# Kernel optimization log

Hardware: AMD Instinct MI355X
Metric: run time of the kernel (lower is better)

## Reference

```python
import jax, jax.numpy as jnp
import numpy as np

M1, M2, BS = 2000, 400, 8
AT = M1 + M2
E1, E2, E3 = 60000, 20000, 20000
H, F, NG, L, C = 64, 64, 50, 4, 4
CUTOFF = 10.0
LOG2 = 0.6931471805599453  # shift of ShiftedSoftplus


def _ssp(x):
    return jax.nn.softplus(x) - LOG2


def _smear(d):
    # GaussianSmearing(0, cutoff, NG)
    offset = jnp.linspace(0.0, CUTOFF, NG)
    coeff = -0.5 / (offset[1] - offset[0]) ** 2
    return jnp.exp(coeff * (d[:, None] - offset[None, :]) ** 2)  # [E, NG]


def _colored_mlp(attr, colors, w1, b1, w2, b2):
    # w1:[C,NG,F] b1:[C,F] w2:[C,F,F] b2:[C,F]; route each edge through its color's MLP
    out = jnp.zeros((attr.shape[0], w1.shape[-1]), attr.dtype)
    for c in range(C):  # fixed small color count
        h = _ssp(attr @ w1[c] + b1[c]) @ w2[c] + b2[c]
        out = out + jnp.where((colors == c)[:, None], h, jnp.zeros((), attr.dtype))
    return out


def _block(h, ei, ew, attr, col, p):
    # InteractionBlock: CFConv -> ssp -> linear
    mw1, mb1, mw2, mb2, cw1, cw2, cb2, bw, bb = p
    Ccut = 0.5 * (jnp.cos(ew * jnp.pi / CUTOFF) + 1.0)
    W = _colored_mlp(attr, col, mw1, mb1, mw2, mb2) * Ccut[:, None]  # [E,F]
    x = h @ cw1                                   # lin1 (no bias) [N,F]
    msg = x[ei[:, 0]] * W                         # gather x_j, modulate
    agg = jax.ops.segment_sum(msg, ei[:, 1], num_segments=h.shape[0])  # scatter-add
    x = agg @ cw2 + cb2                           # lin2
    return _ssp(x) @ bw + bb                      # act + block linear


def _batch_graph(ei, ew, col):
    # replicate per-structure edges across the batch with node offset b*AT
    offs = (jnp.arange(BS, dtype=ei.dtype) * AT)[:, None, None]
    ei_b = (ei[None] + offs).reshape(-1, 2)
    return ei_b, jnp.tile(ew, BS), jnp.tile(col, BS)


def _forward(sites, sites_p, e1, ew1, c1, e2, ew2, c2, e3, ew3, c3,
             emb_w, emb_p_w, mlp_w1, mlp_b1, mlp_w2, mlp_b2,
             conv_w1, conv_w2, conv_b2, blk_w, blk_b,
             out_w1, out_b1, out_w2, out_b2):
    h = jnp.concatenate([emb_w[sites], emb_p_w[sites_p]], axis=1).reshape(BS * AT, H)
    graphs = []
    for (ei, ew, col) in ((e1, ew1, c1), (e2, ew2, c2), (e3, ew3, c3)):
        ei_b, ew_b, col_b = _batch_graph(ei, ew, col)
        graphs.append((ei_b, ew_b, col_b, _smear(ew_b)))
    for l in range(L):
        delta = jnp.zeros_like(h)
        for g, (ei_b, ew_b, col_b, attr_b) in enumerate(graphs):
            p = (mlp_w1[l, g], mlp_b1[l, g], mlp_w2[l, g], mlp_b2[l, g],
                 conv_w1[l, g], conv_w2[l, g], conv_b2[l, g], blk_w[l, g], blk_b[l, g])
            delta = delta + _block(h, ei_b, ew_b, attr_b, col_b, p)
        h = h + delta
    hp = h.reshape(BS, AT, H)[:, M1:, :]   # mask selects pore nodes only
    o = hp @ out_w1 + out_b1               # NB: original has `h - self.act(h)` no-op, so no activation here
    o = o @ out_w2 + out_b2                # [BS, M2, 1]
    return o.sum(axis=1)                   # 'add' readout per batch -> [BS, 1]


def setup_inputs() -> dict:
    key = jax.random.key(0)
    ks = jax.random.split(key, 24)
    f = lambda i, shape, s=0.1: jax.random.normal(ks[i], shape, jnp.float32) * s
    sites = jax.random.randint(ks[0], (BS, M1), 0, 1, dtype=jnp.int32)
    sites_p = jax.random.randint(ks[1], (BS, M2), 0, 2, dtype=jnp.int32)
    e1 = jax.random.randint(ks[2], (E1, 2), 0, M1, dtype=jnp.int32)
    e2 = jnp.stack([jax.random.randint(ks[3], (E2,), 0, M1, dtype=jnp.int32),
                    jax.random.randint(ks[4], (E2,), M1, AT, dtype=jnp.int32)], 1)
    e3 = jnp.stack([jax.random.randint(ks[5], (E3,), M1, AT, dtype=jnp.int32),
                    jax.random.randint(ks[6], (E3,), 0, M1, dtype=jnp.int32)], 1)
    ew1 = jax.random.uniform(ks[7], (E1,), jnp.float32, 0.5, CUTOFF)
    ew2 = jax.random.uniform(ks[8], (E2,), jnp.float32, 0.5, CUTOFF)
    ew3 = jax.random.uniform(ks[9], (E3,), jnp.float32, 0.5, CUTOFF)
    c1 = jax.random.randint(ks[10], (E1,), 0, C, dtype=jnp.int32)
    c2 = jax.random.randint(ks[11], (E2,), 0, C, dtype=jnp.int32)
    c3 = jax.random.randint(ks[12], (E3,), 0, C, dtype=jnp.int32)
    return {
        'sites': sites, 'sites_p': sites_p,
        'edge_idx1': e1, 'edge_weight1': ew1, 'colors1': c1,
        'edge_idx2': e2, 'edge_weight2': ew2, 'colors2': c2,
        'edge_idx3': e3, 'edge_weight3': ew3, 'colors3': c3,
        'emb_w': f(13, (1, H), 1.0), 'emb_p_w': f(14, (2, H), 1.0),
        'mlp_w1': f(15, (L, 3, C, NG, F)), 'mlp_b1': jnp.zeros((L, 3, C, F), jnp.float32),
        'mlp_w2': f(16, (L, 3, C, F, F)), 'mlp_b2': jnp.zeros((L, 3, C, F), jnp.float32),
        'conv_w1': f(17, (L, 3, H, F)), 'conv_w2': f(18, (L, 3, F, H)),
        'conv_b2': jnp.zeros((L, 3, H), jnp.float32),
        'blk_w': f(19, (L, 3, H, H)), 'blk_b': jnp.zeros((L, 3, H), jnp.float32),
        'out_w1': f(20, (H, H // 2)), 'out_b1': jnp.zeros((H // 2,), jnp.float32),
        'out_w2': f(21, (H // 2, 1)), 'out_b2': jnp.zeros((1,), jnp.float32),
    }


def reference(sites, sites_p, edge_idx1, edge_weight1, colors1,
              edge_idx2, edge_weight2, colors2, edge_idx3, edge_weight3, colors3,
              emb_w, emb_p_w, mlp_w1, mlp_b1, mlp_w2, mlp_b2,
              conv_w1, conv_w2, conv_b2, blk_w, blk_b,
              out_w1, out_b1, out_w2, out_b2):
    return _forward(sites, sites_p, edge_idx1, edge_weight1, colors1,
                    edge_idx2, edge_weight2, colors2, edge_idx3, edge_weight3, colors3,
                    emb_w, emb_p_w, mlp_w1, mlp_b1, mlp_w2, mlp_b2,
                    conv_w1, conv_w2, conv_b2, blk_w, blk_b,
                    out_w1, out_b1, out_w2, out_b2)
```

## Files before the change

### kernel.cpp

```cpp
#include <hip/hip_runtime.h>
#include <math.h>

constexpr int M1 = 2000, M2 = 400, BS = 8;
constexpr int AT = M1 + M2;
constexpr int NN = BS * AT;
constexpr int E1 = 60000, E2 = 20000, E3 = 20000;
constexpr int ET = E1 + E2 + E3;
constexpr int H = 64, F = 64, NG = 50, L = 4, C = 4;
constexpr float CUTOFF = 10.0f;
constexpr float LOG2F_ = 0.6931471805599453f;

constexpr float SMEAR_STEP = 10.0f / 49.0f;
constexpr float SMEAR_COEFF = -12.005f;
constexpr float PI_OVER_CUT = 0.31415926535897932f;

constexpr int NBLK = (ET + 255) / 256;

constexpr int NT = 256;
constexpr float DSCALE = (float)(NT - 1) / CUTOFF;

constexpr int TILE_M = 32;

constexpr int SITE_T = M1 / 4;
constexpr int PORE_T = M2 / 4;
constexpr int NBLK_L = 2 * (SITE_T + PORE_T);

constexpr int LT0 = M1 / 4;
constexpr int LT1 = M1 / 4;
constexpr int LT2 = M2 / 4;
constexpr int LTOT = LT0 + LT1 + LT2;

constexpr int A_TAB  = 192;
constexpr int A_INIT = NN * 64 / 256;
constexpr int A_CNT  = NBLK;
constexpr int A_CV   = 3;
constexpr int A_TOT  = A_TAB + A_INIT + A_CNT + A_CV;
constexpr int B_PACK = 48 * NT * 64 / 256;
constexpr int B_TOT  = B_PACK + 3 + 2;

constexpr size_t O_HA    = 0;
constexpr size_t O_HB    = O_HA  + (size_t)NN * 64 * 4;
constexpr size_t O_XG    = O_HB  + (size_t)NN * 64 * 4;
constexpr size_t O_DG    = O_XG  + (size_t)3 * AT * 512 * 2;
constexpr size_t O_TAB2  = O_DG  + (size_t)3 * NN * 64 * 4;
constexpr size_t O_EDATA = O_TAB2 + (size_t)48 * NT * 64 * 4;
constexpr size_t O_INT   = O_EDATA + (size_t)ET * 16;
constexpr int I_DEG  = 0;
constexpr int I_CUR  = 7200;
constexpr int I_ZEND = 14400;
constexpr int I_BASE = 14400;
constexpr int I_PERM = 21616;
constexpr int I_CV   = 26016;

__device__ inline float sspf(float x) {
    return fmaxf(x, 0.0f) + log1pf(expf(-fabsf(x))) - LOG2F_;
}
__device__ inline float sspf_fast(float x) {
    float t = __expf(-fabsf(x));
    return fmaxf(x, 0.0f) + __logf(1.0f + t) - LOG2F_;
}

__device__ inline unsigned int bf16rn(float x) {
    unsigned int u = __float_as_uint(x);
    u = (u + 0x7FFFu + ((u >> 16) & 1u)) >> 16;
    return u & 0xFFFFu;
}

__device__ inline int graph_off(int g) { return g == 0 ? 0 : (g == 1 ? E1 : E1 + E2); }

__device__ inline void edge_decode(int idx, int& g, int& e,
                                   const int* ei1, const int* ei2, const int* ei3,
                                   const int* c1, const int* c2, const int* c3,
                                   const int*& ei, const int*& cl) {
    if (idx < E1)            { g = 0; e = idx;           ei = ei1; cl = c1; }
    else if (idx < E1 + E2)  { g = 1; e = idx - E1;      ei = ei2; cl = c2; }
    else                     { g = 2; e = idx - E1 - E2; ei = ei3; cl = c3; }
}

__global__ __launch_bounds__(256) void k_setupA(
    const float* __restrict__ mlp_w1, const float* __restrict__ mlp_b1,
    const float* __restrict__ mlp_w2, const float* __restrict__ mlp_b2,
    float* __restrict__ tabF,
    const int* __restrict__ sites, const int* __restrict__ sites_p,
    const float* __restrict__ emb_w, const float* __restrict__ emb_p_w,
    float* __restrict__ h,
    const int* __restrict__ ei1, const int* __restrict__ ei2,
    const int* __restrict__ ei3, const int* __restrict__ c1,
    const int* __restrict__ c2, const int* __restrict__ c3,
    int* __restrict__ deg,
    const float* __restrict__ conv_b2, const float* __restrict__ blk_w,
    const float* __restrict__ blk_b, float* __restrict__ cvbuf) {
    int bid = blockIdx.x;
    int t = threadIdx.x;
    if (bid < A_TAB) {
        const int lane = t & 63;
        int wslot = bid * 4 + (t >> 6);
        int s = wslot >> 4;
        int pq = wslot & 15;
        int l = s % L;
        int gc = s / L;
        int c = gc % C;
        int g = gc / C;
        size_t wb = (size_t)((l * 3 + g) * C + c);
        const float* w1 = mlp_w1 + wb * NG * F;
        const float* w2 = mlp_w2 + wb * F * F;
        float w1c[NG], w2c[F];
        #pragma unroll
        for (int k = 0; k < NG; k++) w1c[k] = w1[k * F + lane];
        #pragma unroll
        for (int k = 0; k < F; k++) w2c[k] = w2[k * F + lane];
        float b1c = mlp_b1[wb * F + lane];
        float b2c = mlp_b2[wb * F + lane];
        for (int pp = 0; pp < 16; pp++) {
            int p = pq * 16 + pp;
            float d = (float)p * (CUTOFF / (float)(NT - 1));
            float dd = d - (float)lane * SMEAR_STEP;
            float av = (lane < NG) ? __expf(SMEAR_COEFF * dd * dd) : 0.0f;
            float acc = b1c;
            #pragma unroll
            for (int k = 0; k < NG; k++) acc = fmaf(__shfl(av, k), w1c[k], acc);
            float tt = sspf_fast(acc);
            float acc2 = b2c;
            #pragma unroll
            for (int j = 0; j < F; j++) acc2 = fmaf(__shfl(tt, j), w2c[j], acc2);
            float ccut = 0.5f * (__cosf(d * PI_OVER_CUT) + 1.0f);
            tabF[((size_t)s * NT + p) * 64 + lane] = acc2 * ccut;
        }
    } else if (bid < A_TAB + A_INIT) {
        int idx = (bid - A_TAB) * 256 + t;
        int f = idx & 63;
        int n = idx >> 6;
        int b = n / AT;
        int i = n - b * AT;
        float v;
        if (i < M1) v = emb_w[sites[b * M1 + i] * H + f];
        else        v = emb_p_w[sites_p[b * M2 + (i - M1)] * H + f];
        h[idx] = v;
    } else if (bid < A_TAB + A_INIT + A_CNT) {
        int idx = (bid - A_TAB - A_INIT) * 256 + t;
        if (idx < ET) {
            int g, e; const int* ei; const int* cl;
            edge_decode(idx, g, e, ei1, ei2, ei3, c1, c2, c3, ei, cl);
            atomicAdd(&deg[g * AT + ei[2 * e + 1]], 1);
        }
    } else {
        int s = (bid - A_TAB - A_INIT - A_CNT) * 4 + (t >> 6);
        int lane = t & 63;
        if (s < 12) {
            float sl = sspf(conv_b2[s * 64 + lane]);
            const float* bw = blk_w + (size_t)s * 4096;
            float a = blk_b[s * 64 + lane];
            #pragma unroll 8
            for (int k = 0; k < 64; k++)
                a = fmaf(__shfl(sl, k), bw[k * 64 + lane], a);
            cvbuf[s * 64 + lane] = a;
        }
    }
}

__global__ __launch_bounds__(256) void k_setupB(
    const float* __restrict__ tabF, unsigned int* __restrict__ tab2,
    const int* __restrict__ deg, int* __restrict__ base,
    int* __restrict__ perm) {
    int bid = blockIdx.x;
    int t = threadIdx.x;
    if (bid < B_PACK) {
        int idx = bid * 256 + t;
        int pc = idx & (NT * 64 - 1);
        int nxt = (pc < (NT - 1) * 64) ? idx + 64 : idx;
        unsigned int lo = bf16rn(tabF[idx]);
        unsigned int hi = bf16rn(tabF[nxt]);
        tab2[idx] = lo | (hi << 16);
    } else if (bid < B_PACK + 3) {
        const int T = 256, CH = 10;
        __shared__ int lsum[256];
        int g = bid - B_PACK;
        int loc[CH];
        int s = 0;
        #pragma unroll
        for (int i = 0; i < CH; i++) {
            int idx = t * CH + i;
            int v = (idx < AT) ? deg[g * AT + idx] : 0;
            loc[i] = s;
            s += v;
        }
        lsum[t] = s;
        __syncthreads();
        for (int off = 1; off < T; off <<= 1) {
            int v = 0;
            if (t >= off) v = lsum[t - off];
            __syncthreads();
            lsum[t] += v;
            __syncthreads();
        }
        int tb = lsum[t] - s;
        #pragma unroll
        for (int i = 0; i < CH; i++) {
            int idx = t * CH + i;
            if (idx < AT) base[g * (AT + 1) + idx] = tb + loc[i];
        }
        if (t == T - 1) base[g * (AT + 1) + AT] = lsum[T - 1];
    } else {
        __shared__ int hist[256];
        __shared__ int cur[256];
        int q = bid - B_PACK - 3;
        int cnt   = q ? M2 : M1;
        int obase = q ? M1 : 0;
        hist[t] = 0;
        __syncthreads();
        for (int i = t; i < cnt; i += 256) {
            int key = q ? deg[AT + M1 + i] : (deg[i] + deg[2 * AT + i]);
            atomicAdd(&hist[min(key, 255)], 1);
        }
        __syncthreads();
        if (t == 0) {
            int run = 0;
            for (int k = 0; k < 256; k++) { cur[k] = run; run += hist[k]; }
        }
        __syncthreads();
        for (int i = t; i < cnt; i += 256) {
            int key = q ? deg[AT + M1 + i] : (deg[i] + deg[2 * AT + i]);
            int pos = atomicAdd(&cur[min(key, 255)], 1);
            perm[obase + pos] = q ? (M1 + i) : i;
        }
    }
}

__device__ inline void fma4(float acc[4], float a, const float4 b) {
    acc[0] = fmaf(a, b.x, acc[0]);
    acc[1] = fmaf(a, b.y, acc[1]);
    acc[2] = fmaf(a, b.z, acc[2]);
    acc[3] = fmaf(a, b.w, acc[3]);
}

__device__ inline void stage_B(const float* __restrict__ gB, float (*Bs)[68], int t) {
    #pragma unroll
    for (int i = 0; i < 4; i++) {
        int v = t + i * 256;
        int r = v >> 4, c4 = (v & 15) * 4;
        *(float4*)&Bs[r][c4] = *(const float4*)(gB + (size_t)r * 64 + c4);
    }
}
__device__ inline void gemm_tile(const float (*As)[68], const float (*Bs)[68],
                                 int r0, int c0, float acc0[4], float acc1[4]) {
    #pragma unroll 4
    for (int k0 = 0; k0 < 64; k0 += 4) {
        float4 a0 = *(const float4*)&As[r0][k0];
        float4 a1 = *(const float4*)&As[r0 + 1][k0];
        float4 b0 = *(const float4*)&Bs[k0][c0];
        float4 b1 = *(const float4*)&Bs[k0 + 1][c0];
        float4 b2 = *(const float4*)&Bs[k0 + 2][c0];
        float4 b3 = *(const float4*)&Bs[k0 + 3][c0];
        fma4(acc0, a0.x, b0); fma4(acc0, a0.y, b1);
        fma4(acc0, a0.z, b2); fma4(acc0, a0.w, b3);
        fma4(acc1, a1.x, b0); fma4(acc1, a1.y, b1);
        fma4(acc1, a1.z, b2); fma4(acc1, a1.w, b3);
    }
}
__device__ inline void gemm_row(const float (*As)[68], const float (*Bs)[68],
                                int r, int c0, float acc[4]) {
    #pragma unroll 4
    for (int k0 = 0; k0 < 64; k0 += 4) {
        float4 a = *(const float4*)&As[r][k0];
        float4 b0 = *(const float4*)&Bs[k0][c0];
        float4 b1 = *(const float4*)&Bs[k0 + 1][c0];
        float4 b2 = *(const float4*)&Bs[k0 + 2][c0];
        float4 b3 = *(const float4*)&Bs[k0 + 3][c0];
        fma4(acc, a.x, b0); fma4(acc, a.y, b1);
        fma4(acc, a.z, b2); fma4(acc, a.w, b3);
    }
}

__device__ inline void xg_store8(const float (*T)[68],
                                 unsigned short* __restrict__ xg,
                                 int g, int i0, int t) {
    int k = t >> 6, c = t & 63;
    unsigned int w0 = bf16rn(T[k * 8 + 0][c]) | (bf16rn(T[k * 8 + 1][c]) << 16);
    unsigned int w1 = bf16rn(T[k * 8 + 2][c]) | (bf16rn(T[k * 8 + 3][c]) << 16);
    unsigned int w2 = bf16rn(T[k * 8 + 4][c]) | (bf16rn(T[k * 8 + 5][c]) << 16);
    unsigned int w3 = bf16rn(T[k * 8 + 6][c]) | (bf16rn(T[k * 8 + 7][c]) << 16);
    unsigned short* o0 = xg + (((size_t)(g * 2 + 0) * AT + i0 + k) * 64 + c) * 4;
    unsigned short* o1 = xg + (((size_t)(g * 2 + 1) * AT + i0 + k) * 64 + c) * 4;
    *(uint2*)o0 = make_uint2(w0, w1);
    *(uint2*)o1 = make_uint2(w2, w3);
}
__device__ inline void xg_store4(const float (*T)[68],
                                 unsigned short* __restrict__ xg,
                                 int g, int bh, const int* __restrict__ perm,
                                 int pbase, int gi, int t) {
    int k = t >> 6, c = t & 63;
    int node = perm[pbase + gi * 4 + k];
    unsigned int w0 = bf16rn(T[k * 4 + 0][c]) | (bf16rn(T[k * 4 + 1][c]) << 16);
    unsigned int w1 = bf16rn(T[k * 4 + 2][c]) | (bf16rn(T[k * 4 + 3][c]) << 16);
    unsigned short* out = xg + (((size_t)(g * 2 + bh) * AT + node) * 64 + c) * 4;
    *(uint2*)out = make_uint2(w0, w1);
}

__device__ inline float tab_lerp(unsigned int u, int z) {
    float lo = __uint_as_float(u << 16);
    float hi = __uint_as_float(u & 0xFFFF0000u);
    return fmaf(__int_as_float(z), hi - lo, lo);
}
__device__ inline void gmadd(float acc[4], uint2 q, float wl) {
    acc[0] = fmaf(__uint_as_float(q.x << 16),         wl, acc[0]);
    acc[1] = fmaf(__uint_as_float(q.x & 0xFFFF0000u), wl, acc[1]);
    acc[2] = fmaf(__uint_as_float(q.y << 16),         wl, acc[2]);
    acc[3] = fmaf(__uint_as_float(q.y & 0xFFFF0000u), wl, acc[3]);
}

__device__ inline void gather4(const int4* __restrict__ ed, int s, int e,
                               const unsigned int* __restrict__ tg,
                               const unsigned short* __restrict__ xgg,
                               int lane, float acc[4]) {
    int i = s;
    while (i < e) {
        int cnt = min(e - i, 64);
        int4 mrec = ed[i + min(lane, cnt - 1)];
        int j = 0;
        for (; j + 4 <= cnt; j += 4) {
            int x0 = __shfl(mrec.x, j),     y0 = __shfl(mrec.y, j),     z0 = __shfl(mrec.z, j);
            int x1 = __shfl(mrec.x, j + 1), y1 = __shfl(mrec.y, j + 1), z1 = __shfl(mrec.z, j + 1);
            int x2 = __shfl(mrec.x, j + 2), y2 = __shfl(mrec.y, j + 2), z2 = __shfl(mrec.z, j + 2);
            int x3 = __shfl(mrec.x, j + 3), y3 = __shfl(mrec.y, j + 3), z3 = __shfl(mrec.z, j + 3);
            unsigned int u0 = tg[(size_t)y0 * 64 + lane];
            unsigned int u1 = tg[(size_t)y1 * 64 + lane];
            unsigned int u2 = tg[(size_t)y2 * 64 + lane];
            unsigned int u3 = tg[(size_t)y3 * 64 + lane];
            uint2 q0 = *(const uint2*)(xgg + ((size_t)x0 << 8) + lane * 4);
            uint2 q1 = *(const uint2*)(xgg + ((size_t)x1 << 8) + lane * 4);
            uint2 q2 = *(const uint2*)(xgg + ((size_t)x2 << 8) + lane * 4);
            uint2 q3 = *(const uint2*)(xgg + ((size_t)x3 << 8) + lane * 4);
            float wl0 = tab_lerp(u0, z0);
            float wl1 = tab_lerp(u1, z1);
            float wl2 = tab_lerp(u2, z2);
            float wl3 = tab_lerp(u3, z3);
            gmadd(acc, q0, wl0); gmadd(acc, q1, wl1);
            gmadd(acc, q2, wl2); gmadd(acc, q3, wl3);
        }
        for (; j < cnt; j++) {
            int x0 = __shfl(mrec.x, j), y0 = __shfl(mrec.y, j), z0 = __shfl(mrec.z, j);
            unsigned int u0 = tg[(size_t)y0 * 64 + lane];
            uint2 q0 = *(const uint2*)(xgg + ((size_t)x0 << 8) + lane * 4);
            gmadd(acc, q0, tab_lerp(u0, z0));
        }
        i += cnt;
    }
}

__global__ __launch_bounds__(256) void k_layer(
    const int4* __restrict__ edata, const int* __restrict__ base,
    const int* __restrict__ perm,
    unsigned short* __restrict__ xg, const unsigned int* __restrict__ tab2,
    const float* __restrict__ conv_w2, const float* __restrict__ conv_b2,
    const float* __restrict__ blk_w, const float* __restrict__ blk_b,
    const float* __restrict__ conv_w1, const float* __restrict__ cvbuf,
    const float* __restrict__ hIn, float* __restrict__ hOut,
    int l, int last) {
    __shared__ float As[16][68];
    __shared__ float Ps[16][68];
    __shared__ float Bs[64][68];
    const int t = threadIdx.x;
    const int lane = t & 63;
    const int wv = t >> 6;
    int bid = blockIdx.x;
    int site, tile, bh;
    if (bid < 2 * SITE_T) { site = 1; tile = bid >> 1; bh = bid & 1; }
    else { site = 0; tile = (bid - 2 * SITE_T) >> 1; bh = (bid - 2 * SITE_T) & 1; }
    const int gi = site ? (SITE_T - 1 - tile) : (PORE_T - 1 - tile);
    const int pbperm = site ? 0 : M1;
    const int gA = site ? 0 : 1;
    const size_t pbA = (size_t)(l * 3 + gA);
    const size_t pbB = (size_t)(l * 3 + 2);

    stage_B(conv_w2 + pbA * 4096, Bs, t);

    const int dst = perm[pbperm + gi * 4 + wv];
    float accA[4] = {0, 0, 0, 0}, accB[4] = {0, 0, 0, 0};
    {
        int s = base[gA * (AT + 1) + dst];
        int e = base[gA * (AT + 1) + dst + 1];
        gather4(edata + graph_off(gA), s, e,
                tab2 + ((size_t)gA * C * L + l) * NT * 64,
                xg + (size_t)(gA * 2 + bh) * AT * 256, lane, accA);
    }
    if (site) {
        int s = base[2 * (AT + 1) + dst];
        int e = base[2 * (AT + 1) + dst + 1];
        gather4(edata + graph_off(2), s, e,
                tab2 + ((size_t)2 * C * L + l) * NT * 64,
                xg + (size_t)(2 * 2 + bh) * AT * 256, lane, accB);
    }
    #pragma unroll
    for (int b = 0; b < 4; b++) As[wv * 4 + b][lane] = accA[b];
    __syncthreads();

    const int r = t >> 4;
    const int c0 = (t & 15) * 4;
    const int k = r >> 2, bl = r & 3;
    const int node = perm[pbperm + gi * 4 + k];
    const int batch = bh * 4 + bl;
    const size_t o = ((size_t)batch * AT + node) * 64 + c0;
    const float* cvl = cvbuf + (size_t)l * 3 * 64;

    float4 cb = *(const float4*)(conv_b2 + pbA * 64 + c0);
    float x[4] = {cb.x, cb.y, cb.z, cb.w};
    gemm_row(As, Bs, r, c0, x);
    __syncthreads();
    *(float4*)&As[r][c0] =
        make_float4(sspf(x[0]), sspf(x[1]), sspf(x[2]), sspf(x[3]));
    stage_B(blk_w + pbA * 4096, Bs, t);
    __syncthreads();

    float4 hv = *(const float4*)(hIn + o);
    float4 bbA = *(const float4*)(blk_b + pbA * 64 + c0);
    float d[4];
    if (site) {
        float4 bbB = *(const float4*)(blk_b + pbB * 64 + c0);
        float4 cv1 = *(const float4*)(cvl + 64 + c0);
        d[0] = hv.x + bbA.x + bbB.x + cv1.x;
        d[1] = hv.y + bbA.y + bbB.y + cv1.y;
        d[2] = hv.z + bbA.z + bbB.z + cv1.z;
        d[3] = hv.w + bbA.w + bbB.w + cv1.w;
    } else {
        float4 cv0 = *(const float4*)(cvl + c0);
        float4 cv2 = *(const float4*)(cvl + 128 + c0);
        d[0] = hv.x + bbA.x + cv0.x + cv2.x;
        d[1] = hv.y + bbA.y + cv0.y + cv2.y;
        d[2] = hv.z + bbA.z + cv0.z + cv2.z;
        d[3] = hv.w + bbA.w + cv0.w + cv2.w;
    }
    gemm_row(As, Bs, r, c0, d);
    if (site) {
        __syncthreads();
        #pragma unroll
        for (int b = 0; b < 4; b++) As[wv * 4 + b][lane] = accB[b];
        stage_B(conv_w2 + pbB * 4096, Bs, t);
        __syncthreads();
        float4 cb2v = *(const float4*)(conv_b2 + pbB * 64 + c0);
        float y[4] = {cb2v.x, cb2v.y, cb2v.z, cb2v.w};
        gemm_row(As, Bs, r, c0, y);
        __syncthreads();
        *(float4*)&As[r][c0] =
            make_float4(sspf(y[0]), sspf(y[1]), sspf(y[2]), sspf(y[3]));
        stage_B(blk_w + pbB * 4096, Bs, t);
        __syncthreads();
        gemm_row(As, Bs, r, c0, d);
    }
    *(float4*)(hOut + o) = make_float4(d[0], d[1], d[2], d[3]);
    if (last) return;

    __syncthreads();
    *(float4*)&As[r][c0] = make_float4(d[0], d[1], d[2], d[3]);
    stage_B(conv_w1 + (size_t)((l + 1) * 3 + (site ? 0 : 2)) * 4096, Bs, t);
    __syncthreads();
    float p[4] = {0, 0, 0, 0};
    gemm_row(As, Bs, r, c0, p);
    __syncthreads();
    *(float4*)&Ps[r][c0] = make_float4(p[0], p[1], p[2], p[3]);
    if (site) stage_B(conv_w1 + (size_t)((l + 1) * 3 + 1) * 4096, Bs, t);
    __syncthreads();
    xg_store4(Ps, xg, site ? 0 : 2, bh, perm, pbperm, gi, t);
    if (site) {
        float q[4] = {0, 0, 0, 0};
        gemm_row(As, Bs, r, c0, q);
        __syncthreads();
        *(float4*)&Ps[r][c0] = make_float4(q[0], q[1], q[2], q[3]);
        __syncthreads();
        xg_store4(Ps, xg, 1, bh, perm, pbperm, gi, t);
    }
}

__global__ __launch_bounds__(256) void k_fl(
    const int* __restrict__ ei1, const int* __restrict__ ei2,
    const int* __restrict__ ei3, const int* __restrict__ c1,
    const int* __restrict__ c2, const int* __restrict__ c3,
    const float* __restrict__ ew1, const float* __restrict__ ew2,
    const float* __restrict__ ew3,
    const int* __restrict__ base, int* __restrict__ cur,
    int4* __restrict__ edata,
    const float* __restrict__ h, const float* __restrict__ conv_w1,
    unsigned short* __restrict__ xg) {
    __shared__ float As[TILE_M][68];
    __shared__ float Bs[64][68];
    int t = threadIdx.x;
    if (blockIdx.x >= LTOT) {
        int idx = (blockIdx.x - LTOT) * 256 + t;
        if (idx >= ET) return;
        int g, e; const int* ei; const int* cl;
        edge_decode(idx, g, e, ei1, ei2, ei3, c1, c2, c3, ei, cl);
        const float* ew = (g == 0) ? ew1 : (g == 1 ? ew2 : ew3);
        int dst = ei[2 * e + 1];
        int src = ei[2 * e];
        int p = base[g * (AT + 1) + dst] + atomicAdd(&cur[g * AT + dst], 1);
        float tt = ew[e] * DSCALE;
        int i0 = min((int)tt, NT - 2);
        float fr = tt - (float)i0;
        int cb = cl[e] * (L * NT) + i0;
        edata[graph_off(g) + p] = make_int4(src, cb, __float_as_int(fr), 0);
        return;
    }
    int g, igrp;
    {
        int bid = blockIdx.x;
        if (bid < LT0)            { g = 0; igrp = bid; }
        else if (bid < LT0 + LT1) { g = 1; igrp = bid - LT0; }
        else                      { g = 2; igrp = LT0 + (bid - LT0 - LT1); }
    }
    int i0 = igrp * 4;
    #pragma unroll
    for (int it = 0; it < 2; it++) {
        int v = t + it * 256;
        int r = v >> 4, c4 = (v & 15) * 4;
        int n = (r & 7) * AT + i0 + (r >> 3);
        *(float4*)&As[r][c4] = *(const float4*)(h + (size_t)n * 64 + c4);
    }
    stage_B(conv_w1 + (size_t)g * 4096, Bs, t);
    __syncthreads();
    int cg = t & 15, rg = t >> 4;
    int c0 = cg * 4, r0 = rg * 2;
    float acc0[4] = {0, 0, 0, 0}, acc1[4] = {0, 0, 0, 0};
    gemm_tile(As, Bs, r0, c0, acc0, acc1);
    __syncthreads();
    *(float4*)&As[r0][c0]     = make_float4(acc0[0], acc0[1], acc0[2], acc0[3]);
    *(float4*)&As[r0 + 1][c0] = make_float4(acc1[0], acc1[1], acc1[2], acc1[3]);
    __syncthreads();
    xg_store8(As, xg, g, i0, t);
}

__global__ void k_read(const float* __restrict__ h,
                       const float* __restrict__ w1, const float* __restrict__ b1,
                       const float* __restrict__ w2, const float* __restrict__ b2,
                       float* __restrict__ out) {
    int b = blockIdx.x;
    int lane = threadIdx.x & 63;
    int wv = threadIdx.x >> 6;
    __shared__ float part[4];
    float weff = 0.0f;
    #pragma unroll
    for (int j = 0; j < H / 2; j++) weff = fmaf(w1[lane * (H / 2) + j], w2[j], weff);
    float acc = 0.0f;
    for (int i = wv * (M2 / 4); i < (wv + 1) * (M2 / 4); i++)
        acc += h[((size_t)b * AT + M1 + i) * H + lane];
    float v = acc * weff;
    for (int off = 32; off; off >>= 1) v += __shfl_xor(v, off);
    if (lane == 0) part[wv] = v;
    __syncthreads();
    if (threadIdx.x == 0) {
        float bias = b2[0];
        for (int j = 0; j < H / 2; j++) bias = fmaf(b1[j], w2[j], bias);
        out[b] = part[0] + part[1] + part[2] + part[3] + (float)M2 * bias;
    }
}

extern "C" void kernel_launch(void* const* d_in, const int* in_sizes, int n_in,
                              void* d_out, int out_size, void* d_ws, size_t ws_size,
                              hipStream_t stream) {
    const int* sites   = (const int*)d_in[0];
    const int* sites_p = (const int*)d_in[1];
    const int* ei1 = (const int*)d_in[2];
    const float* ew1 = (const float*)d_in[3];
    const int* c1 = (const int*)d_in[4];
    const int* ei2 = (const int*)d_in[5];
    const float* ew2 = (const float*)d_in[6];
    const int* c2 = (const int*)d_in[7];
    const int* ei3 = (const int*)d_in[8];
    const float* ew3 = (const float*)d_in[9];
    const int* c3 = (const int*)d_in[10];
    const float* emb_w   = (const float*)d_in[11];
    const float* emb_p_w = (const float*)d_in[12];
    const float* mlp_w1 = (const float*)d_in[13];
    const float* mlp_b1 = (const float*)d_in[14];
    const float* mlp_w2 = (const float*)d_in[15];
    const float* mlp_b2 = (const float*)d_in[16];
    const float* conv_w1 = (const float*)d_in[17];
    const float* conv_w2 = (const float*)d_in[18];
    const float* conv_b2 = (const float*)d_in[19];
    const float* blk_w = (const float*)d_in[20];
    const float* blk_b = (const float*)d_in[21];
    const float* out_w1 = (const float*)d_in[22];
    const float* out_b1 = (const float*)d_in[23];
    const float* out_w2 = (const float*)d_in[24];
    const float* out_b2 = (const float*)d_in[25];

    char* ws = (char*)d_ws;
    float* hA   = (float*)(ws + O_HA);
    float* hB   = (float*)(ws + O_HB);
    unsigned short* xg = (unsigned short*)(ws + O_XG);
    float* tabF = (float*)(ws + O_DG);
    unsigned int* tab2 = (unsigned int*)(ws + O_TAB2);
    int4*  edata = (int4*)(ws + O_EDATA);
    int* ip    = (int*)(ws + O_INT);
    int* deg   = ip + I_DEG;
    int* cur   = ip + I_CUR;
    int* ibase = ip + I_BASE;
    int* dperm = ip + I_PERM;
    float* cvbuf = (float*)(ip + I_CV);

    hipMemsetAsync(ip, 0, (size_t)I_ZEND * sizeof(int), stream);

    k_setupA<<<A_TOT, 256, 0, stream>>>(mlp_w1, mlp_b1, mlp_w2, mlp_b2, tabF,
                                        sites, sites_p, emb_w, emb_p_w, hA,
                                        ei1, ei2, ei3, c1, c2, c3, deg,
                                        conv_b2, blk_w, blk_b, cvbuf);
    k_setupB<<<B_TOT, 256, 0, stream>>>(tabF, tab2, deg, ibase, dperm);
    k_fl<<<LTOT + NBLK, 256, 0, stream>>>(ei1, ei2, ei3, c1, c2, c3,
                                          ew1, ew2, ew3, ibase, cur, edata,
                                          hA, conv_w1, xg);

    float* hcur = hA;
    float* hnxt = hB;
    for (int l = 0; l < L; l++) {
        int last = (l == L - 1) ? 1 : 0;
        k_layer<<<NBLK_L, 256, 0, stream>>>(edata, ibase, dperm, xg, tab2,
                                            conv_w2, conv_b2, blk_w, blk_b,
                                            conv_w1, cvbuf, hcur, hnxt, l, last);
        float* tmp = hcur; hcur = hnxt; hnxt = tmp;
    }
    k_read<<<BS, 256, 0, stream>>>(hcur, out_w1, out_b1, out_w2, out_b2, (float*)d_out);
}
```

Measured before the change: 323.6 us.

## Pad edge lists to multiples of four, store xg in fp32, prefetch weights

Pads each destination's CSR edge segment up to a multiple of four using dummy edges whose table entry is zero. This lets the gather loop read edge records directly in groups of four instead of using a wave-wide load plus shuffles and a remainder loop. Node features xg are now stored as fp32 rather than packed bf16, which removes the conversion but doubles gather bandwidth. Weight tiles for the next GEMM stage are loaded into registers ahead of time so global latency overlaps with compute, and the loop bounds are made wave-uniform with readfirstlane. The risks are extra memory traffic from the fp32 features and the padding, and the dummy edges rely on the table's last entry producing a zero weight.

```diff
diff --git a/kernel.cpp b/kernel.cpp
--- a/kernel.cpp
+++ b/kernel.cpp
@@ -19,6 +19,11 @@
 constexpr int NT = 256;
 constexpr float DSCALE = (float)(NT - 1) / CUTOFF;
 
+constexpr int GP0 = E1 + 3 * M1;
+constexpr int GP1 = E2 + 3 * M2;
+constexpr int GP2 = E3 + 3 * M1;
+constexpr int ETP = GP0 + GP1 + GP2;
+
 constexpr int TILE_M = 32;
 
 constexpr int SITE_T = M1 / 4;
@@ -29,6 +34,7 @@
 constexpr int LT1 = M1 / 4;
 constexpr int LT2 = M2 / 4;
 constexpr int LTOT = LT0 + LT1 + LT2;
+constexpr int PADB = (3 * AT + 255) / 256;
 
 constexpr int A_TAB  = 192;
 constexpr int A_INIT = NN * 64 / 256;
@@ -41,10 +47,10 @@
 constexpr size_t O_HA    = 0;
 constexpr size_t O_HB    = O_HA  + (size_t)NN * 64 * 4;
 constexpr size_t O_XG    = O_HB  + (size_t)NN * 64 * 4;
-constexpr size_t O_DG    = O_XG  + (size_t)3 * AT * 512 * 2;
-constexpr size_t O_TAB2  = O_DG  + (size_t)3 * NN * 64 * 4;
+constexpr size_t O_TABF  = O_XG  + (size_t)3 * 2 * AT * 256 * 4;
+constexpr size_t O_TAB2  = O_TABF + (size_t)48 * NT * 64 * 4;
 constexpr size_t O_EDATA = O_TAB2 + (size_t)48 * NT * 64 * 4;
-constexpr size_t O_INT   = O_EDATA + (size_t)ET * 16;
+constexpr size_t O_INT   = O_EDATA + (size_t)ETP * 16;
 constexpr int I_DEG  = 0;
 constexpr int I_CUR  = 7200;
 constexpr int I_ZEND = 14400;
@@ -66,7 +72,7 @@
     return u & 0xFFFFu;
 }
 
-__device__ inline int graph_off(int g) { return g == 0 ? 0 : (g == 1 ? E1 : E1 + E2); }
+__device__ inline int graph_off(int g) { return g == 0 ? 0 : (g == 1 ? GP0 : GP0 + GP1); }
 
 __device__ inline void edge_decode(int idx, int& g, int& e,
                                    const int* ei1, const int* ei2, const int* ei3,
@@ -180,7 +186,7 @@
         #pragma unroll
         for (int i = 0; i < CH; i++) {
             int idx = t * CH + i;
-            int v = (idx < AT) ? deg[g * AT + idx] : 0;
+            int v = (idx < AT) ? ((deg[g * AT + idx] + 3) & ~3) : 0;
             loc[i] = s;
             s += v;
         }
@@ -241,6 +247,24 @@
         *(float4*)&Bs[r][c4] = *(const float4*)(gB + (size_t)r * 64 + c4);
     }
 }
+struct WReg { float4 v0, v1, v2, v3; };
+__device__ inline WReg stage_ld(const float* __restrict__ g, int t) {
+    int r0 = t >> 4, c4 = (t & 15) * 4;
+    WReg w;
+    w.v0 = *(const float4*)(g + (size_t)r0 * 64 + c4);
+    w.v1 = *(const float4*)(g + (size_t)(r0 + 16) * 64 + c4);
+    w.v2 = *(const float4*)(g + (size_t)(r0 + 32) * 64 + c4);
+    w.v3 = *(const float4*)(g + (size_t)(r0 + 48) * 64 + c4);
+    return w;
+}
+__device__ inline void stage_st(const WReg& w, float (*Bs)[68], int t) {
+    int r0 = t >> 4, c4 = (t & 15) * 4;
+    *(float4*)&Bs[r0][c4]      = w.v0;
+    *(float4*)&Bs[r0 + 16][c4] = w.v1;
+    *(float4*)&Bs[r0 + 32][c4] = w.v2;
+    *(float4*)&Bs[r0 + 48][c4] = w.v3;
+}
+
 __device__ inline void gemm_tile(const float (*As)[68], const float (*Bs)[68],
                                  int r0, int c0, float acc0[4], float acc1[4]) {
     #pragma unroll 4
@@ -271,29 +295,24 @@
     }
 }
 
-__device__ inline void xg_store8(const float (*T)[68],
-                                 unsigned short* __restrict__ xg,
+__device__ inline void xg_store8(const float (*T)[68], float* __restrict__ xg,
                                  int g, int i0, int t) {
     int k = t >> 6, c = t & 63;
-    unsigned int w0 = bf16rn(T[k * 8 + 0][c]) | (bf16rn(T[k * 8 + 1][c]) << 16);
-    unsigned int w1 = bf16rn(T[k * 8 + 2][c]) | (bf16rn(T[k * 8 + 3][c]) << 16);
-    unsigned int w2 = bf16rn(T[k * 8 + 4][c]) | (bf16rn(T[k * 8 + 5][c]) << 16);
-    unsigned int w3 = bf16rn(T[k * 8 + 6][c]) | (bf16rn(T[k * 8 + 7][c]) << 16);
-    unsigned short* o0 = xg + (((size_t)(g * 2 + 0) * AT + i0 + k) * 64 + c) * 4;
-    unsigned short* o1 = xg + (((size_t)(g * 2 + 1) * AT + i0 + k) * 64 + c) * 4;
-    *(uint2*)o0 = make_uint2(w0, w1);
-    *(uint2*)o1 = make_uint2(w2, w3);
-}
-__device__ inline void xg_store4(const float (*T)[68],
-                                 unsigned short* __restrict__ xg,
+    float* o0 = xg + (((size_t)(g * 2 + 0) * AT + i0 + k) * 64 + c) * 4;
+    float* o1 = xg + (((size_t)(g * 2 + 1) * AT + i0 + k) * 64 + c) * 4;
+    *(float4*)o0 = make_float4(T[k * 8 + 0][c], T[k * 8 + 1][c],
+                               T[k * 8 + 2][c], T[k * 8 + 3][c]);
+    *(float4*)o1 = make_float4(T[k * 8 + 4][c], T[k * 8 + 5][c],
+                               T[k * 8 + 6][c], T[k * 8 + 7][c]);
+}
+__device__ inline void xg_store4(const float (*T)[68], float* __restrict__ xg,
                                  int g, int bh, const int* __restrict__ perm,
                                  int pbase, int gi, int t) {
     int k = t >> 6, c = t & 63;
     int node = perm[pbase + gi * 4 + k];
-    unsigned int w0 = bf16rn(T[k * 4 + 0][c]) | (bf16rn(T[k * 4 + 1][c]) << 16);
-    unsigned int w1 = bf16rn(T[k * 4 + 2][c]) | (bf16rn(T[k * 4 + 3][c]) << 16);
-    unsigned short* out = xg + (((size_t)(g * 2 + bh) * AT + node) * 64 + c) * 4;
-    *(uint2*)out = make_uint2(w0, w1);
+    float* out = xg + (((size_t)(g * 2 + bh) * AT + node) * 64 + c) * 4;
+    *(float4*)out = make_float4(T[k * 4 + 0][c], T[k * 4 + 1][c],
+                                T[k * 4 + 2][c], T[k * 4 + 3][c]);
 }
 
 __device__ inline float tab_lerp(unsigned int u, int z) {
@@ -301,56 +320,39 @@
     float hi = __uint_as_float(u & 0xFFFF0000u);
     return fmaf(__int_as_float(z), hi - lo, lo);
 }
-__device__ inline void gmadd(float acc[4], uint2 q, float wl) {
-    acc[0] = fmaf(__uint_as_float(q.x << 16),         wl, acc[0]);
-    acc[1] = fmaf(__uint_as_float(q.x & 0xFFFF0000u), wl, acc[1]);
-    acc[2] = fmaf(__uint_as_float(q.y << 16),         wl, acc[2]);
-    acc[3] = fmaf(__uint_as_float(q.y & 0xFFFF0000u), wl, acc[3]);
-}
 
 __device__ inline void gather4(const int4* __restrict__ ed, int s, int e,
                                const unsigned int* __restrict__ tg,
-                               const unsigned short* __restrict__ xgg,
+                               const float* __restrict__ xgg,
                                int lane, float acc[4]) {
-    int i = s;
-    while (i < e) {
-        int cnt = min(e - i, 64);
-        int4 mrec = ed[i + min(lane, cnt - 1)];
-        int j = 0;
-        for (; j + 4 <= cnt; j += 4) {
-            int x0 = __shfl(mrec.x, j),     y0 = __shfl(mrec.y, j),     z0 = __shfl(mrec.z, j);
-            int x1 = __shfl(mrec.x, j + 1), y1 = __shfl(mrec.y, j + 1), z1 = __shfl(mrec.z, j + 1);
-            int x2 = __shfl(mrec.x, j + 2), y2 = __shfl(mrec.y, j + 2), z2 = __shfl(mrec.z, j + 2);
-            int x3 = __shfl(mrec.x, j + 3), y3 = __shfl(mrec.y, j + 3), z3 = __shfl(mrec.z, j + 3);
-            unsigned int u0 = tg[(size_t)y0 * 64 + lane];
-            unsigned int u1 = tg[(size_t)y1 * 64 + lane];
-            unsigned int u2 = tg[(size_t)y2 * 64 + lane];
-            unsigned int u3 = tg[(size_t)y3 * 64 + lane];
-            uint2 q0 = *(const uint2*)(xgg + ((size_t)x0 << 8) + lane * 4);
-            uint2 q1 = *(const uint2*)(xgg + ((size_t)x1 << 8) + lane * 4);
-            uint2 q2 = *(const uint2*)(xgg + ((size_t)x2 << 8) + lane * 4);
-            uint2 q3 = *(const uint2*)(xgg + ((size_t)x3 << 8) + lane * 4);
-            float wl0 = tab_lerp(u0, z0);
-            float wl1 = tab_lerp(u1, z1);
-            float wl2 = tab_lerp(u2, z2);
-            float wl3 = tab_lerp(u3, z3);
-            gmadd(acc, q0, wl0); gmadd(acc, q1, wl1);
-            gmadd(acc, q2, wl2); gmadd(acc, q3, wl3);
-        }
-        for (; j < cnt; j++) {
-            int x0 = __shfl(mrec.x, j), y0 = __shfl(mrec.y, j), z0 = __shfl(mrec.z, j);
-            unsigned int u0 = tg[(size_t)y0 * 64 + lane];
-            uint2 q0 = *(const uint2*)(xgg + ((size_t)x0 << 8) + lane * 4);
-            gmadd(acc, q0, tab_lerp(u0, z0));
-        }
-        i += cnt;
+    for (int i = s; i < e; i += 4) {
+        int4 e0 = ed[i];
+        int4 e1 = ed[i + 1];
+        int4 e2 = ed[i + 2];
+        int4 e3 = ed[i + 3];
+        unsigned int u0 = tg[(size_t)e0.y * 64 + lane];
+        unsigned int u1 = tg[(size_t)e1.y * 64 + lane];
+        unsigned int u2 = tg[(size_t)e2.y * 64 + lane];
+        unsigned int u3 = tg[(size_t)e3.y * 64 + lane];
+        float4 q0 = *(const float4*)(xgg + ((size_t)e0.x << 8) + lane * 4);
+        float4 q1 = *(const float4*)(xgg + ((size_t)e1.x << 8) + lane * 4);
+        float4 q2 = *(const float4*)(xgg + ((size_t)e2.x << 8) + lane * 4);
+        float4 q3 = *(const float4*)(xgg + ((size_t)e3.x << 8) + lane * 4);
+        float wl0 = tab_lerp(u0, e0.z);
+        float wl1 = tab_lerp(u1, e1.z);
+        float wl2 = tab_lerp(u2, e2.z);
+        float wl3 = tab_lerp(u3, e3.z);
+        fma4(acc, wl0, q0);
+        fma4(acc, wl1, q1);
+        fma4(acc, wl2, q2);
+        fma4(acc, wl3, q3);
     }
 }
 
 __global__ __launch_bounds__(256) void k_layer(
     const int4* __restrict__ edata, const int* __restrict__ base,
     const int* __restrict__ perm,
-    unsigned short* __restrict__ xg, const unsigned int* __restrict__ tab2,
+    float* __restrict__ xg, const unsigned int* __restrict__ tab2,
     const float* __restrict__ conv_w2, const float* __restrict__ conv_b2,
     const float* __restrict__ blk_w, const float* __restrict__ blk_b,
     const float* __restrict__ conv_w1, const float* __restrict__ cvbuf,
@@ -372,26 +374,28 @@
     const size_t pbA = (size_t)(l * 3 + gA);
     const size_t pbB = (size_t)(l * 3 + 2);
 
-    stage_B(conv_w2 + pbA * 4096, Bs, t);
-
-    const int dst = perm[pbperm + gi * 4 + wv];
+    WReg R = stage_ld(conv_w2 + pbA * 4096, t);
+
+    const int dst = __builtin_amdgcn_readfirstlane(perm[pbperm + gi * 4 + wv]);
     float accA[4] = {0, 0, 0, 0}, accB[4] = {0, 0, 0, 0};
     {
-        int s = base[gA * (AT + 1) + dst];
-        int e = base[gA * (AT + 1) + dst + 1];
+        int s = __builtin_amdgcn_readfirstlane(base[gA * (AT + 1) + dst]);
+        int e = __builtin_amdgcn_readfirstlane(base[gA * (AT + 1) + dst + 1]);
         gather4(edata + graph_off(gA), s, e,
                 tab2 + ((size_t)gA * C * L + l) * NT * 64,
                 xg + (size_t)(gA * 2 + bh) * AT * 256, lane, accA);
     }
     if (site) {
-        int s = base[2 * (AT + 1) + dst];
-        int e = base[2 * (AT + 1) + dst + 1];
+        int s = __builtin_amdgcn_readfirstlane(base[2 * (AT + 1) + dst]);
+        int e = __builtin_amdgcn_readfirstlane(base[2 * (AT + 1) + dst + 1]);
         gather4(edata + graph_off(2), s, e,
                 tab2 + ((size_t)2 * C * L + l) * NT * 64,
                 xg + (size_t)(2 * 2 + bh) * AT * 256, lane, accB);
     }
     #pragma unroll
     for (int b = 0; b < 4; b++) As[wv * 4 + b][lane] = accA[b];
+    stage_st(R, Bs, t);
+    R = stage_ld(blk_w + pbA * 4096, t);
     __syncthreads();
 
     const int r = t >> 4;
@@ -408,7 +412,9 @@
     __syncthreads();
     *(float4*)&As[r][c0] =
         make_float4(sspf(x[0]), sspf(x[1]), sspf(x[2]), sspf(x[3]));
-    stage_B(blk_w + pbA * 4096, Bs, t);
+    stage_st(R, Bs, t);
+    if (site) R = stage_ld(conv_w2 + pbB * 4096, t);
+    else if (!last) R = stage_ld(conv_w1 + (size_t)((l + 1) * 3 + 2) * 4096, t);
     __syncthreads();
 
     float4 hv = *(const float4*)(hIn + o);
@@ -434,7 +440,8 @@
         __syncthreads();
         #pragma unroll
         for (int b = 0; b < 4; b++) As[wv * 4 + b][lane] = accB[b];
-        stage_B(conv_w2 + pbB * 4096, Bs, t);
+        stage_st(R, Bs, t);
+        R = stage_ld(blk_w + pbB * 4096, t);
         __syncthreads();
         float4 cb2v = *(const float4*)(conv_b2 + pbB * 64 + c0);
         float y[4] = {cb2v.x, cb2v.y, cb2v.z, cb2v.w};
@@ -442,7 +449,8 @@
         __syncthreads();
         *(float4*)&As[r][c0] =
             make_float4(sspf(y[0]), sspf(y[1]), sspf(y[2]), sspf(y[3]));
-        stage_B(blk_w + pbB * 4096, Bs, t);
+        stage_st(R, Bs, t);
+        if (!last) R = stage_ld(conv_w1 + (size_t)((l + 1) * 3 + 0) * 4096, t);
         __syncthreads();
         gemm_row(As, Bs, r, c0, d);
     }
@@ -451,13 +459,14 @@
 
     __syncthreads();
     *(float4*)&As[r][c0] = make_float4(d[0], d[1], d[2], d[3]);
-    stage_B(conv_w1 + (size_t)((l + 1) * 3 + (site ? 0 : 2)) * 4096, Bs, t);
+    stage_st(R, Bs, t);
+    if (site) R = stage_ld(conv_w1 + (size_t)((l + 1) * 3 + 1) * 4096, t);
     __syncthreads();
     float p[4] = {0, 0, 0, 0};
     gemm_row(As, Bs, r, c0, p);
     __syncthreads();
     *(float4*)&Ps[r][c0] = make_float4(p[0], p[1], p[2], p[3]);
-    if (site) stage_B(conv_w1 + (size_t)((l + 1) * 3 + 1) * 4096, Bs, t);
+    if (site) stage_st(R, Bs, t);
     __syncthreads();
     xg_store4(Ps, xg, site ? 0 : 2, bh, perm, pbperm, gi, t);
     if (site) {
@@ -477,12 +486,22 @@
     const float* __restrict__ ew1, const float* __restrict__ ew2,
     const float* __restrict__ ew3,
     const int* __restrict__ base, int* __restrict__ cur,
-    int4* __restrict__ edata,
+    const int* __restrict__ deg, int4* __restrict__ edata,
     const float* __restrict__ h, const float* __restrict__ conv_w1,
-    unsigned short* __restrict__ xg) {
+    float* __restrict__ xg) {
     __shared__ float As[TILE_M][68];
     __shared__ float Bs[64][68];
     int t = threadIdx.x;
+    if (blockIdx.x >= LTOT + NBLK) {
+        int idx = (blockIdx.x - LTOT - NBLK) * 256 + t;
+        if (idx >= 3 * AT) return;
+        int g = idx / AT, dn = idx - g * AT;
+        int d = deg[g * AT + dn];
+        int pd = (d + 3) & ~3;
+        int4* ep = edata + graph_off(g) + base[g * (AT + 1) + dn] + d;
+        for (int k2 = 0; k2 < pd - d; k2++) ep[k2] = make_int4(0, NT - 1, 0, 0);
+        return;
+    }
     if (blockIdx.x >= LTOT) {
         int idx = (blockIdx.x - LTOT) * 256 + t;
         if (idx >= ET) return;
@@ -585,8 +604,8 @@
     char* ws = (char*)d_ws;
     float* hA   = (float*)(ws + O_HA);
     float* hB   = (float*)(ws + O_HB);
-    unsigned short* xg = (unsigned short*)(ws + O_XG);
-    float* tabF = (float*)(ws + O_DG);
+    float* xg   = (float*)(ws + O_XG);
+    float* tabF = (float*)(ws + O_TABF);
     unsigned int* tab2 = (unsigned int*)(ws + O_TAB2);
     int4*  edata = (int4*)(ws + O_EDATA);
     int* ip    = (int*)(ws + O_INT);
@@ -603,9 +622,9 @@
                                         ei1, ei2, ei3, c1, c2, c3, deg,
                                         conv_b2, blk_w, blk_b, cvbuf);
     k_setupB<<<B_TOT, 256, 0, stream>>>(tabF, tab2, deg, ibase, dperm);
-    k_fl<<<LTOT + NBLK, 256, 0, stream>>>(ei1, ei2, ei3, c1, c2, c3,
-                                          ew1, ew2, ew3, ibase, cur, edata,
-                                          hA, conv_w1, xg);
+    k_fl<<<LTOT + NBLK + PADB, 256, 0, stream>>>(ei1, ei2, ei3, c1, c2, c3,
+                                                 ew1, ew2, ew3, ibase, cur, deg,
+                                                 edata, hA, conv_w1, xg);
 
     float* hcur = hA;
     float* hnxt = hB;
```

Result: no change. 324.8 us (+0.4%).
